# Performance work log

Hardware: AMD Instinct MI355X
Metric: run time of the kernel (lower is better)

The kernel has to match this reference:

```python
import jax, jax.numpy as jnp
import numpy as np
import math

D_MODEL = 1024
D_STATE = 16
D_CONV = 4
EXPAND = 2
D_INNER = EXPAND * D_MODEL  # 2048
DT_RANK = 64
B_SZ = 2
L_SEQ = 1024


def setup_inputs() -> dict:
    key = jax.random.key(0)
    ks = jax.random.split(key, 10)
    x = jax.random.normal(ks[0], (B_SZ, L_SEQ, D_MODEL), dtype=jnp.float32)
    in_proj_w = jax.random.normal(ks[1], (2 * D_INNER, D_MODEL), dtype=jnp.float32) * (1.0 / math.sqrt(D_MODEL))
    conv_w = jax.random.normal(ks[2], (D_INNER, 1, D_CONV), dtype=jnp.float32) * (1.0 / math.sqrt(D_CONV))
    conv_b = jax.random.normal(ks[3], (D_INNER,), dtype=jnp.float32) * 0.01
    x_proj_w = jax.random.normal(ks[4], (DT_RANK + 2 * D_STATE, D_INNER), dtype=jnp.float32) * (1.0 / math.sqrt(D_INNER))
    dt_init_std = DT_RANK ** (-0.5)
    dt_proj_w = jax.random.uniform(ks[5], (D_INNER, DT_RANK), dtype=jnp.float32, minval=-dt_init_std, maxval=dt_init_std)
    dt = jnp.exp(jax.random.uniform(ks[6], (D_INNER,), dtype=jnp.float32) * (math.log(0.1) - math.log(0.001)) + math.log(0.001))
    dt = jnp.clip(dt, 1e-4, None)
    dt_proj_b = dt + jnp.log(-jnp.expm1(-dt))
    A_log = jnp.log(jnp.tile(jnp.arange(1, D_STATE + 1, dtype=jnp.float32)[None, :], (D_INNER, 1)))
    D = jnp.ones((D_INNER,), dtype=jnp.float32)
    out_proj_w = jax.random.normal(ks[7], (D_MODEL, D_INNER), dtype=jnp.float32) * (1.0 / math.sqrt(D_INNER))
    return {"x": x, "in_proj_w": in_proj_w, "conv_w": conv_w, "conv_b": conv_b,
            "x_proj_w": x_proj_w, "dt_proj_w": dt_proj_w, "dt_proj_b": dt_proj_b,
            "A_log": A_log, "D": D, "out_proj_w": out_proj_w}


def _mamba_forward(x, in_proj_w, conv_w, conv_b, x_proj_w, dt_proj_w, dt_proj_b, A_log, D, out_proj_w):
    B, L, _ = x.shape
    # input projection -> x, z each [B, L, Di]
    xz = jnp.einsum('bld,ed->ble', x, in_proj_w)
    xs, z = jnp.split(xz, 2, axis=-1)
    # causal depthwise conv along L (torch pads K-1 both sides then trims -> left pad only)
    xc = jnp.transpose(xs, (0, 2, 1))  # [B, Di, L]
    xc = jax.lax.conv_general_dilated(
        xc, conv_w, window_strides=(1,), padding=[(D_CONV - 1, 0)],
        feature_group_count=D_INNER, dimension_numbers=('NCH', 'OIH', 'NCH'))
    xc = xc + conv_b[None, :, None]
    xs = jnp.transpose(xc, (0, 2, 1))  # [B, L, Di]
    xs = jax.nn.silu(xs)
    # SSM parameters
    A = -jnp.exp(A_log)  # [Di, N]
    dbc = jnp.einsum('bld,ed->ble', xs, x_proj_w)
    delta_r = dbc[..., :DT_RANK]
    Bm = dbc[..., DT_RANK:DT_RANK + D_STATE]       # [B, L, N]
    Cm = dbc[..., DT_RANK + D_STATE:]              # [B, L, N]
    delta = jnp.einsum('blr,dr->bld', delta_r, dt_proj_w)
    delta = jax.nn.softplus(delta + dt_proj_b)     # [B, L, Di]
    # selective scan: h_t = exp(delta*A)*h_{t-1} + delta*B*x
    dA = jnp.exp(delta[..., None] * A)                          # [B, L, Di, N]
    dBx = (delta * xs)[..., None] * Bm[:, :, None, :]           # [B, L, Di, N]
    dA_t = jnp.moveaxis(dA, 1, 0)    # [L, B, Di, N]
    dBx_t = jnp.moveaxis(dBx, 1, 0)
    C_t = jnp.moveaxis(Cm, 1, 0)     # [L, B, N]
    h0 = jnp.zeros((B, D_INNER, D_STATE), dtype=xs.dtype)

    def step(h, inp):
        da, bx, c = inp
        h = da * h + bx
        y = jnp.einsum('bdn,bn->bd', h, c)
        return h, y

    _, ys = jax.lax.scan(step, h0, (dA_t, dBx_t, C_t))
    y = jnp.moveaxis(ys, 0, 1)       # [B, L, Di]
    y = y + D * xs
    # gating and output projection
    out = y * jax.nn.silu(z)
    return jnp.einsum('bld,od->blo', out, out_proj_w)


def reference(x, in_proj_w, conv_w, conv_b, x_proj_w, dt_proj_w, dt_proj_b, A_log, D, out_proj_w):
    return _mamba_forward(x, in_proj_w, conv_w, conv_b, x_proj_w, dt_proj_w, dt_proj_b, A_log, D, out_proj_w)
```

## Files before the change

### kernel.cpp

```cpp
#include <hip/hip_runtime.h>
#include <hip/hip_bf16.h>

typedef __attribute__((ext_vector_type(8))) short short8;
typedef __attribute__((ext_vector_type(4))) float f32x4;
typedef __hip_bfloat16 bf16;

#define D_MODEL 1024
#define D_INNER 2048
#define DT_RANK 64
#define D_STATE 16
#define B_SZ 2
#define L_SEQ 1024
#define NSEG 32
#define SL 32

__device__ __forceinline__ float b2f(bf16 x){ return __bfloat162float(x); }
__device__ __forceinline__ bf16  f2b(float x){ return __float2bfloat16(x); }

__device__ __forceinline__ void cvt_store8(bf16* dst, const float* s){
  union { short8 v; bf16 e[8]; } u;
  #pragma unroll
  for (int i = 0; i < 8; i++) u.e[i] = f2b(s[i]);
  *(short8*)dst = u.v;
}

__device__ __forceinline__ void gl_lds16(const bf16* g, bf16* l){
  __builtin_amdgcn_global_load_lds((const __attribute__((address_space(1))) unsigned int*)g,
                                   (__attribute__((address_space(3))) unsigned int*)l, 16, 0, 0);
}

__global__ __launch_bounds__(256) void cvt5_k(const float* s0, bf16* d0, int c0,
                                              const float* s1, bf16* d1, int c1,
                                              const float* s2, bf16* d2, int c2,
                                              const float* s3, bf16* d3, int c3,
                                              const float* s4, bf16* d4, int c4)
{
  int i = blockIdx.x * 256 + threadIdx.x;
  const float* s; bf16* d; int off;
  if      (i < c0) { s = s0; d = d0; off = i; }
  else if (i < c1) { s = s1; d = d1; off = i - c0; }
  else if (i < c2) { s = s2; d = d2; off = i - c1; }
  else if (i < c3) { s = s3; d = d3; off = i - c2; }
  else if (i < c4) { s = s4; d = d4; off = i - c3; }
  else return;
  float b[8];
  *(float4*)&b[0] = *(const float4*)(s + (size_t)off * 8);
  *(float4*)&b[4] = *(const float4*)(s + (size_t)off * 8 + 4);
  cvt_store8(d + (size_t)off * 8, b);
}

template<int MODE, int JT, int SPLITK>
__global__ __launch_bounds__(256) void gemm_glds(const bf16* __restrict__ A,
                                                 const bf16* __restrict__ B,
                                                 void* __restrict__ Cout,
                                                 int M, int N, int K)
{
  constexpr int BN = JT * 32;
  constexpr int BI = BN / 64;
  __shared__ bf16 As[128 * 32];
  __shared__ bf16 Bs[BN * 32];

  const int gx = gridDim.x;
  const int nwg = gx * gridDim.y;
  const int flat = blockIdx.y * gx + blockIdx.x;
  const int swz = (flat & 7) * (nwg >> 3) + (flat >> 3);
  const int bm = (swz / gx) * 128, bn = (swz % gx) * BN;

  const int Kc = K / SPLITK;
  const int kb = (SPLITK > 1) ? blockIdx.z * Kc : 0;

  const int tid  = threadIdx.x;
  const int lane = tid & 63, wave = tid >> 6;
  const int wm = (wave & 1) * 64, wn = (wave >> 1) * (JT * 16);
  const int r = lane & 15, q = lane >> 4;

  const bf16* asrc[2];
  #pragma unroll
  for (int i = 0; i < 2; i++) {
    int c = i * 256 + tid;
    asrc[i] = A + (size_t)(bm + (c >> 2)) * K + kb + (c & 3) * 8;
  }
  const bf16* bsrc[BI];
  #pragma unroll
  for (int i = 0; i < BI; i++) {
    int c = i * 256 + tid;
    bsrc[i] = B + (size_t)(bn + (c >> 2)) * K + kb + (c & 3) * 8;
  }

  f32x4 acc[4][JT];
  #pragma unroll
  for (int i = 0; i < 4; i++)
    #pragma unroll
    for (int j = 0; j < JT; j++) acc[i][j] = (f32x4){0.f,0.f,0.f,0.f};

  for (int k0 = 0; k0 < Kc; k0 += 32) {
    #pragma unroll
    for (int i = 0; i < 2; i++)
      gl_lds16(asrc[i] + k0, &As[(i * 256 + tid) * 8]);
    #pragma unroll
    for (int i = 0; i < BI; i++)
      gl_lds16(bsrc[i] + k0, &Bs[(i * 256 + tid) * 8]);
    __syncthreads();
    short8 af[4], bfr[JT];
    #pragma unroll
    for (int i = 0; i < 4; i++)  af[i]  = *(const short8*)&As[(wm + i*16 + r) * 32 + q*8];
    #pragma unroll
    for (int j = 0; j < JT; j++) bfr[j] = *(const short8*)&Bs[(wn + j*16 + r) * 32 + q*8];
    #pragma unroll
    for (int j = 0; j < JT; j++)
      #pragma unroll
      for (int i = 0; i < 4; i++)
        acc[i][j] = __builtin_amdgcn_mfma_f32_16x16x32_bf16(af[i], bfr[j], acc[i][j], 0, 0, 0);
    __syncthreads();
  }

  float* outf = (float*)Cout + (size_t)((SPLITK > 1) ? blockIdx.z : 0) * M * N;
  #pragma unroll
  for (int i = 0; i < 4; i++)
    #pragma unroll
    for (int j = 0; j < JT; j++)
      #pragma unroll
      for (int t = 0; t < 4; t++) {
        int row = bm + wm + i*16 + q*4 + t;
        int col = bn + wn + j*16 + r;
        float v = acc[i][j][t];
        if (MODE == 0) outf[(size_t)row * N + col] = v;
        else           ((bf16*)Cout)[(size_t)row * N + col] = f2b(v);
      }
}

__global__ __launch_bounds__(256) void addout_k(const float* __restrict__ p,
                                                float* __restrict__ out, int n4)
{
  int i = blockIdx.x * 256 + threadIdx.x;
  float4 a = ((const float4*)p)[i];
  float4 b = ((const float4*)p)[(size_t)i + n4];
  float4 o; o.x = a.x + b.x; o.y = a.y + b.y; o.z = a.z + b.z; o.w = a.w + b.w;
  ((float4*)out)[i] = o;
}

__global__ __launch_bounds__(256) void gemm_dt(const bf16* __restrict__ A,
                                               const bf16* __restrict__ W,
                                               float* __restrict__ Cout,
                                               const float* __restrict__ bias,
                                               int M, int N)
{
  __shared__ __align__(16) float stg[4][16][68];
  const int lane = threadIdx.x & 63, wave = threadIdx.x >> 6;
  const int ntg  = N >> 6;
  const int task = blockIdx.x * 4 + wave;
  const int mt   = task / ntg;
  const int ng   = task - mt * ntg;
  const int r = lane & 15, q = lane >> 4;

  const bf16* pa = A + (size_t)(mt*16 + r) * DT_RANK + q*8;
  short8 a0 = *(const short8*)pa;
  short8 a1 = *(const short8*)(pa + 32);

  #pragma unroll
  for (int j = 0; j < 4; j++) {
    const bf16* pb = W + (size_t)(ng*64 + j*16 + r) * DT_RANK + q*8;
    short8 b0 = *(const short8*)pb;
    short8 b1 = *(const short8*)(pb + 32);
    f32x4 c = {0.f,0.f,0.f,0.f};
    c = __builtin_amdgcn_mfma_f32_16x16x32_bf16(a0, b0, c, 0, 0, 0);
    c = __builtin_amdgcn_mfma_f32_16x16x32_bf16(a1, b1, c, 0, 0, 0);
    float bv = bias[ng*64 + j*16 + r];
    #pragma unroll
    for (int t = 0; t < 4; t++) {
      float xv = c[t] + bv;
      float sp = (xv > 20.f) ? xv : log1pf(__expf(xv));
      stg[wave][q*4 + t][j*16 + r] = sp;
    }
  }
  {
    int row = lane >> 2, q4 = lane & 3;
    const float* src = &stg[wave][row][q4 * 16];
    float4 w0 = *(const float4*)(src);
    float4 w1 = *(const float4*)(src + 4);
    float4 w2 = *(const float4*)(src + 8);
    float4 w3 = *(const float4*)(src + 12);
    float* gdst = Cout + (size_t)(mt*16 + row) * N + ng*64 + q4*16;
    *(float4*)(gdst)      = w0;
    *(float4*)(gdst + 4)  = w1;
    *(float4*)(gdst + 8)  = w2;
    *(float4*)(gdst + 12) = w3;
  }
}

__global__ __launch_bounds__(256) void gemm_xproj(const bf16* __restrict__ A,
                                                  const bf16* __restrict__ W,
                                                  float* __restrict__ dbc,
                                                  bf16* __restrict__ dr)
{
  const int K = D_INNER;
  const int lane = threadIdx.x & 63, wave = threadIdx.x >> 6;
  const int mt = blockIdx.y * 4 + wave;
  const int nt = blockIdx.x;
  const int r = lane & 15, q = lane >> 4;
  const bf16* pa = A + (size_t)(mt*16 + r) * K + q*8;
  const bf16* pb = W + (size_t)(nt*16 + r) * K + q*8;
  f32x4 a0 = {0.f,0.f,0.f,0.f}, a1 = a0, a2 = a0, a3 = a0;
  for (int k0 = 0; k0 < K; k0 += 128) {
    short8 x0 = *(const short8*)(pa + k0);
    short8 w0 = *(const short8*)(pb + k0);
    short8 x1 = *(const short8*)(pa + k0 + 32);
    short8 w1 = *(const short8*)(pb + k0 + 32);
    short8 x2 = *(const short8*)(pa + k0 + 64);
    short8 w2 = *(const short8*)(pb + k0 + 64);
    short8 x3 = *(const short8*)(pa + k0 + 96);
    short8 w3 = *(const short8*)(pb + k0 + 96);
    a0 = __builtin_amdgcn_mfma_f32_16x16x32_bf16(x0, w0, a0, 0, 0, 0);
    a1 = __builtin_amdgcn_mfma_f32_16x16x32_bf16(x1, w1, a1, 0, 0, 0);
    a2 = __builtin_amdgcn_mfma_f32_16x16x32_bf16(x2, w2, a2, 0, 0, 0);
    a3 = __builtin_amdgcn_mfma_f32_16x16x32_bf16(x3, w3, a3, 0, 0, 0);
  }
  f32x4 acc = (a0 + a1) + (a2 + a3);
  #pragma unroll
  for (int t = 0; t < 4; t++) {
    int row = mt*16 + q*4 + t;
    int col = nt*16 + r;
    dbc[(size_t)row * 96 + col] = acc[t];
    if (col < DT_RANK) dr[(size_t)row * DT_RANK + col] = f2b(acc[t]);
  }
}

__global__ __launch_bounds__(256) void conv_silu_k(const bf16* __restrict__ xz,
                                                   const float* __restrict__ cw,
                                                   const float* __restrict__ cb,
                                                   bf16* __restrict__ xs_b)
{
  int idx = blockIdx.x * 256 + threadIdx.x;
  int dg = idx & (D_INNER/8 - 1);
  int bl = idx >> 8;
  int l  = bl & (L_SEQ - 1);
  int d0 = dg * 8;
  const float4* cw4 = (const float4*)cw;
  float4 w[8];
  #pragma unroll
  for (int i = 0; i < 8; i++) w[i] = cw4[d0 + i];
  float acc[8];
  #pragma unroll
  for (int i = 0; i < 8; i++) acc[i] = cb[d0 + i];
  #pragma unroll
  for (int j = 0; j < 4; ++j) {
    int lp = l - 3 + j;
    if (lp >= 0) {
      short8 v = *(const short8*)(xz + (size_t)(bl - 3 + j) * (2*D_INNER) + d0);
      #pragma unroll
      for (int i = 0; i < 8; i++)
        acc[i] += ((const float*)&w[i])[j] * b2f(((const bf16*)&v)[i]);
    }
  }
  float o[8];
  #pragma unroll
  for (int i = 0; i < 8; i++) o[i] = acc[i] / (1.f + __expf(-acc[i]));
  cvt_store8(xs_b + (size_t)idx * 8, o);
}

__global__ __launch_bounds__(256) void scan_pass1(const float* __restrict__ delta,
                                                  const bf16* __restrict__ xs,
                                                  const float* __restrict__ dbc,
                                                  const float* __restrict__ A_log,
                                                  float* __restrict__ hseg,
                                                  float* __restrict__ Stot)
{
  __shared__ float bcs[SL][32];
  const int d   = blockIdx.x * 256 + threadIdx.x;
  const int seg = blockIdx.y, b = blockIdx.z;
  for (int i = threadIdx.x; i < SL*32; i += 256) {
    int l = i >> 5, c = i & 31;
    bcs[l][c] = dbc[((size_t)b*L_SEQ + seg*SL + l)*96 + DT_RANK + c];
  }
  __syncthreads();
  float An[16], h[16];
  #pragma unroll
  for (int n = 0; n < 16; n++) { An[n] = -__expf(A_log[d*16 + n]); h[n] = 0.f; }
  float S = 0.f;
  for (int li = 0; li < SL; ++li) {
    size_t bl = (size_t)b * L_SEQ + seg*SL + li;
    float dv = delta[bl*D_INNER + d];
    float xv = b2f(xs[bl*D_INNER + d]);
    S += dv;
    float dx = dv * xv;
    #pragma unroll
    for (int n = 0; n < 16; n++)
      h[n] = __expf(dv * An[n]) * h[n] + dx * bcs[li][n];
  }
  float* hp = hseg + (((size_t)seg*B_SZ + b)*D_INNER + d) * 16;
  #pragma unroll
  for (int n = 0; n < 16; n++) hp[n] = h[n];
  Stot[((size_t)seg*B_SZ + b)*D_INNER + d] = S;
}

__global__ __launch_bounds__(256) void scan_combine(const float* __restrict__ Stot,
                                                    float* __restrict__ hseg,
                                                    const float* __restrict__ A_log)
{
  int idx = blockIdx.x * 256 + threadIdx.x;
  int n = idx & 15;
  int d = (idx >> 4) & (D_INNER - 1);
  int b = idx >> 15;
  float An = -__expf(A_log[d*16 + n]);
  float H = 0.f;
  for (int s = 0; s < NSEG; s++) {
    size_t base = ((size_t)s*B_SZ + b)*D_INNER + d;
    float St   = Stot[base];
    float hloc = hseg[base*16 + n];
    hseg[base*16 + n] = H;
    H = __expf(An*St)*H + hloc;
  }
}

__global__ __launch_bounds__(256) void scan_pass3(const float* __restrict__ delta,
                                                  const bf16* __restrict__ xs,
                                                  const float* __restrict__ dbc,
                                                  const float* __restrict__ A_log,
                                                  const float* __restrict__ hseg,
                                                  const bf16* __restrict__ xz,
                                                  const float* __restrict__ Dw,
                                                  bf16* __restrict__ outin)
{
  __shared__ float bcs[SL][32];
  const int d   = blockIdx.x * 256 + threadIdx.x;
  const int seg = blockIdx.y, b = blockIdx.z;
  for (int i = threadIdx.x; i < SL*32; i += 256) {
    int l = i >> 5, c = i & 31;
    bcs[l][c] = dbc[((size_t)b*L_SEQ + seg*SL + l)*96 + DT_RANK + c];
  }
  __syncthreads();
  float An[16], h[16];
  const float* hp = hseg + (((size_t)seg*B_SZ + b)*D_INNER + d) * 16;
  #pragma unroll
  for (int n = 0; n < 16; n++) { An[n] = -__expf(A_log[d*16 + n]); h[n] = hp[n]; }
  const float Dv = Dw[d];
  for (int li = 0; li < SL; ++li) {
    size_t bl = (size_t)b * L_SEQ + seg*SL + li;
    float dv = delta[bl*D_INNER + d];
    float xv = b2f(xs[bl*D_INNER + d]);
    float dx = dv * xv;
    float y = 0.f;
    #pragma unroll
    for (int n = 0; n < 16; n++) {
      h[n] = __expf(dv * An[n]) * h[n] + dx * bcs[li][n];
      y   += h[n] * bcs[li][16 + n];
    }
    y += Dv * xv;
    float z = b2f(xz[bl*(size_t)(2*D_INNER) + D_INNER + d]);
    float g = z / (1.f + __expf(-z));
    outin[bl*D_INNER + d] = f2b(y * g);
  }
}

extern "C" void kernel_launch(void* const* d_in, const int* in_sizes, int n_in,
                              void* d_out, int out_size, void* d_ws, size_t ws_size,
                              hipStream_t stream)
{
  const float* x      = (const float*)d_in[0];
  const float* in_w   = (const float*)d_in[1];
  const float* conv_w = (const float*)d_in[2];
  const float* conv_b = (const float*)d_in[3];
  const float* xp_w   = (const float*)d_in[4];
  const float* dt_w   = (const float*)d_in[5];
  const float* dt_b   = (const float*)d_in[6];
  const float* A_log  = (const float*)d_in[7];
  const float* Dw     = (const float*)d_in[8];
  const float* out_w  = (const float*)d_in[9];
  float* out = (float*)d_out;

  char* p = (char*)d_ws;
  bf16*  xz    = (bf16*)p;  p += (size_t)B_SZ*L_SEQ*2*D_INNER*2;
  bf16*  xs_b  = (bf16*)p;  p += (size_t)B_SZ*L_SEQ*D_INNER*2;
  float* dbc   = (float*)p; p += (size_t)B_SZ*L_SEQ*96*4;
  bf16*  dr    = (bf16*)p;  p += (size_t)B_SZ*L_SEQ*DT_RANK*2;
  float* delta = (float*)p; p += (size_t)B_SZ*L_SEQ*D_INNER*4;
  float* Stot  = (float*)p; p += (size_t)NSEG*B_SZ*D_INNER*4;
  bf16*  outin = (bf16*)p;  p += (size_t)B_SZ*L_SEQ*D_INNER*2;
  bf16*  xp_wb = (bf16*)p;  p += (size_t)(DT_RANK+2*D_STATE)*D_INNER*2;
  bf16*  dt_wb = (bf16*)p;  p += (size_t)D_INNER*DT_RANK*2;
  bf16*  ow_b  = (bf16*)p;  p += (size_t)D_MODEL*D_INNER*2;
  float* out_p = (float*)p; p += (size_t)2*B_SZ*L_SEQ*D_MODEL*4;
  char* u = p;
  bf16*  xb    = (bf16*)u;
  bf16*  in_wb = (bf16*)(u + (size_t)B_SZ*L_SEQ*D_MODEL*2);
  float* hseg  = (float*)u;
  p += (size_t)B_SZ*L_SEQ*(D_MODEL + 2*D_INNER)*2;

  const int M = B_SZ * L_SEQ;

  cvt5_k<<<4256, 256, 0, stream>>>(x, xb, 262144,
                                   in_w, in_wb, 786432,
                                   xp_w, xp_wb, 811008,
                                   dt_w, dt_wb, 827392,
                                   out_w, ow_b, 1089536);
  gemm_glds<2,2,1><<<dim3(2*D_INNER/64, M/128, 1), 256, 0, stream>>>(xb, in_wb, xz, M, 2*D_INNER, D_MODEL);
  conv_silu_k<<<(M*D_INNER/8)/256, 256, 0, stream>>>(xz, conv_w, conv_b, xs_b);
  gemm_xproj<<<dim3(6, M/64), 256, 0, stream>>>(xs_b, xp_wb, dbc, dr);
  gemm_dt<<<(M/16)*(D_INNER/64)/4, 256, 0, stream>>>(dr, dt_wb, delta, dt_b, M, D_INNER);
  scan_pass1<<<dim3(D_INNER/256, NSEG, B_SZ), 256, 0, stream>>>(delta, xs_b, dbc, A_log, hseg, Stot);
  scan_combine<<<(B_SZ*D_INNER*16)/256, 256, 0, stream>>>(Stot, hseg, A_log);
  scan_pass3<<<dim3(D_INNER/256, NSEG, B_SZ), 256, 0, stream>>>(delta, xs_b, dbc, A_log, hseg, xz, Dw, outin);
  gemm_glds<0,2,2><<<dim3(D_MODEL/64, M/128, 2), 256, 0, stream>>>(outin, ow_b, out_p, M, D_MODEL, D_INNER);
  addout_k<<<(M*D_MODEL/4)/256, 256, 0, stream>>>(out_p, out, M*D_MODEL/4);
}
```

Before: 261.4 us.

## Specialise scan for integer A via power recurrence and drop split-K output GEMM

Adds a runtime check in both scan passes: when A equals -(n+1) for each state, the per-state decay is computed as successive powers of exp(-delta), replacing sixteen exponentials per step with one exponential and multiplies. The general path remains as a fallback. The output projection GEMM no longer uses split-K with a separate reduction kernel; it writes results directly, saving a partial buffer and an extra pass but halving the grid size. The power recurrence may accumulate slightly more rounding error than direct exponentials.

```diff
diff --git a/kernel.cpp b/kernel.cpp
--- a/kernel.cpp
+++ b/kernel.cpp
@@ -49,7 +49,7 @@
   cvt_store8(d + (size_t)off * 8, b);
 }
 
-template<int MODE, int JT, int SPLITK>
+template<int MODE, int JT>
 __global__ __launch_bounds__(256) void gemm_glds(const bf16* __restrict__ A,
                                                  const bf16* __restrict__ B,
                                                  void* __restrict__ Cout,
@@ -66,9 +66,6 @@
   const int swz = (flat & 7) * (nwg >> 3) + (flat >> 3);
   const int bm = (swz / gx) * 128, bn = (swz % gx) * BN;
 
-  const int Kc = K / SPLITK;
-  const int kb = (SPLITK > 1) ? blockIdx.z * Kc : 0;
-
   const int tid  = threadIdx.x;
   const int lane = tid & 63, wave = tid >> 6;
   const int wm = (wave & 1) * 64, wn = (wave >> 1) * (JT * 16);
@@ -78,13 +75,13 @@
   #pragma unroll
   for (int i = 0; i < 2; i++) {
     int c = i * 256 + tid;
-    asrc[i] = A + (size_t)(bm + (c >> 2)) * K + kb + (c & 3) * 8;
+    asrc[i] = A + (size_t)(bm + (c >> 2)) * K + (c & 3) * 8;
   }
   const bf16* bsrc[BI];
   #pragma unroll
   for (int i = 0; i < BI; i++) {
     int c = i * 256 + tid;
-    bsrc[i] = B + (size_t)(bn + (c >> 2)) * K + kb + (c & 3) * 8;
+    bsrc[i] = B + (size_t)(bn + (c >> 2)) * K + (c & 3) * 8;
   }
 
   f32x4 acc[4][JT];
@@ -93,7 +90,7 @@
     #pragma unroll
     for (int j = 0; j < JT; j++) acc[i][j] = (f32x4){0.f,0.f,0.f,0.f};
 
-  for (int k0 = 0; k0 < Kc; k0 += 32) {
+  for (int k0 = 0; k0 < K; k0 += 32) {
     #pragma unroll
     for (int i = 0; i < 2; i++)
       gl_lds16(asrc[i] + k0, &As[(i * 256 + tid) * 8]);
@@ -114,7 +111,6 @@
     __syncthreads();
   }
 
-  float* outf = (float*)Cout + (size_t)((SPLITK > 1) ? blockIdx.z : 0) * M * N;
   #pragma unroll
   for (int i = 0; i < 4; i++)
     #pragma unroll
@@ -124,19 +120,9 @@
         int row = bm + wm + i*16 + q*4 + t;
         int col = bn + wn + j*16 + r;
         float v = acc[i][j][t];
-        if (MODE == 0) outf[(size_t)row * N + col] = v;
+        if (MODE == 0) ((float*)Cout)[(size_t)row * N + col] = v;
         else           ((bf16*)Cout)[(size_t)row * N + col] = f2b(v);
       }
-}
-
-__global__ __launch_bounds__(256) void addout_k(const float* __restrict__ p,
-                                                float* __restrict__ out, int n4)
-{
-  int i = blockIdx.x * 256 + threadIdx.x;
-  float4 a = ((const float4*)p)[i];
-  float4 b = ((const float4*)p)[(size_t)i + n4];
-  float4 o; o.x = a.x + b.x; o.y = a.y + b.y; o.z = a.z + b.z; o.w = a.w + b.w;
-  ((float4*)out)[i] = o;
 }
 
 __global__ __launch_bounds__(256) void gemm_dt(const bf16* __restrict__ A,
@@ -258,6 +244,13 @@
   cvt_store8(xs_b + (size_t)idx * 8, o);
 }
 
+__device__ __forceinline__ bool an_is_int(const float* An){
+  bool f = true;
+  #pragma unroll
+  for (int n = 0; n < 16; n++) f = f & (fabsf(An[n] + (float)(n+1)) < 1e-3f);
+  return f;
+}
+
 __global__ __launch_bounds__(256) void scan_pass1(const float* __restrict__ delta,
                                                   const bf16* __restrict__ xs,
                                                   const float* __restrict__ dbc,
@@ -277,15 +270,31 @@
   #pragma unroll
   for (int n = 0; n < 16; n++) { An[n] = -__expf(A_log[d*16 + n]); h[n] = 0.f; }
   float S = 0.f;
-  for (int li = 0; li < SL; ++li) {
-    size_t bl = (size_t)b * L_SEQ + seg*SL + li;
-    float dv = delta[bl*D_INNER + d];
-    float xv = b2f(xs[bl*D_INNER + d]);
-    S += dv;
-    float dx = dv * xv;
-    #pragma unroll
-    for (int n = 0; n < 16; n++)
-      h[n] = __expf(dv * An[n]) * h[n] + dx * bcs[li][n];
+  if (an_is_int(An)) {
+    for (int li = 0; li < SL; ++li) {
+      size_t bl = (size_t)b * L_SEQ + seg*SL + li;
+      float dv = delta[bl*D_INNER + d];
+      float xv = b2f(xs[bl*D_INNER + d]);
+      S += dv;
+      float dx = dv * xv;
+      float q = __expf(-dv), w = 1.f;
+      #pragma unroll
+      for (int n = 0; n < 16; n++) {
+        w *= q;
+        h[n] = w * h[n] + dx * bcs[li][n];
+      }
+    }
+  } else {
+    for (int li = 0; li < SL; ++li) {
+      size_t bl = (size_t)b * L_SEQ + seg*SL + li;
+      float dv = delta[bl*D_INNER + d];
+      float xv = b2f(xs[bl*D_INNER + d]);
+      S += dv;
+      float dx = dv * xv;
+      #pragma unroll
+      for (int n = 0; n < 16; n++)
+        h[n] = __expf(dv * An[n]) * h[n] + dx * bcs[li][n];
+    }
   }
   float* hp = hseg + (((size_t)seg*B_SZ + b)*D_INNER + d) * 16;
   #pragma unroll
@@ -334,21 +343,42 @@
   #pragma unroll
   for (int n = 0; n < 16; n++) { An[n] = -__expf(A_log[d*16 + n]); h[n] = hp[n]; }
   const float Dv = Dw[d];
-  for (int li = 0; li < SL; ++li) {
-    size_t bl = (size_t)b * L_SEQ + seg*SL + li;
-    float dv = delta[bl*D_INNER + d];
-    float xv = b2f(xs[bl*D_INNER + d]);
-    float dx = dv * xv;
-    float y = 0.f;
-    #pragma unroll
-    for (int n = 0; n < 16; n++) {
-      h[n] = __expf(dv * An[n]) * h[n] + dx * bcs[li][n];
-      y   += h[n] * bcs[li][16 + n];
-    }
-    y += Dv * xv;
-    float z = b2f(xz[bl*(size_t)(2*D_INNER) + D_INNER + d]);
-    float g = z / (1.f + __expf(-z));
-    outin[bl*D_INNER + d] = f2b(y * g);
+  if (an_is_int(An)) {
+    for (int li = 0; li < SL; ++li) {
+      size_t bl = (size_t)b * L_SEQ + seg*SL + li;
+      float dv = delta[bl*D_INNER + d];
+      float xv = b2f(xs[bl*D_INNER + d]);
+      float dx = dv * xv;
+      float q = __expf(-dv), w = 1.f;
+      float y = 0.f;
+      #pragma unroll
+      for (int n = 0; n < 16; n++) {
+        w *= q;
+        h[n] = w * h[n] + dx * bcs[li][n];
+        y   += h[n] * bcs[li][16 + n];
+      }
+      y += Dv * xv;
+      float z = b2f(xz[bl*(size_t)(2*D_INNER) + D_INNER + d]);
+      float g = z / (1.f + __expf(-z));
+      outin[bl*D_INNER + d] = f2b(y * g);
+    }
+  } else {
+    for (int li = 0; li < SL; ++li) {
+      size_t bl = (size_t)b * L_SEQ + seg*SL + li;
+      float dv = delta[bl*D_INNER + d];
+      float xv = b2f(xs[bl*D_INNER + d]);
+      float dx = dv * xv;
+      float y = 0.f;
+      #pragma unroll
+      for (int n = 0; n < 16; n++) {
+        h[n] = __expf(dv * An[n]) * h[n] + dx * bcs[li][n];
+        y   += h[n] * bcs[li][16 + n];
+      }
+      y += Dv * xv;
+      float z = b2f(xz[bl*(size_t)(2*D_INNER) + D_INNER + d]);
+      float g = z / (1.f + __expf(-z));
+      outin[bl*D_INNER + d] = f2b(y * g);
+    }
   }
 }
 
@@ -379,7 +409,6 @@
   bf16*  xp_wb = (bf16*)p;  p += (size_t)(DT_RANK+2*D_STATE)*D_INNER*2;
   bf16*  dt_wb = (bf16*)p;  p += (size_t)D_INNER*DT_RANK*2;
   bf16*  ow_b  = (bf16*)p;  p += (size_t)D_MODEL*D_INNER*2;
-  float* out_p = (float*)p; p += (size_t)2*B_SZ*L_SEQ*D_MODEL*4;
   char* u = p;
   bf16*  xb    = (bf16*)u;
   bf16*  in_wb = (bf16*)(u + (size_t)B_SZ*L_SEQ*D_MODEL*2);
@@ -393,13 +422,12 @@
                                    xp_w, xp_wb, 811008,
                                    dt_w, dt_wb, 827392,
                                    out_w, ow_b, 1089536);
-  gemm_glds<2,2,1><<<dim3(2*D_INNER/64, M/128, 1), 256, 0, stream>>>(xb, in_wb, xz, M, 2*D_INNER, D_MODEL);
+  gemm_glds<2,2><<<dim3(2*D_INNER/64, M/128), 256, 0, stream>>>(xb, in_wb, xz, M, 2*D_INNER, D_MODEL);
   conv_silu_k<<<(M*D_INNER/8)/256, 256, 0, stream>>>(xz, conv_w, conv_b, xs_b);
   gemm_xproj<<<dim3(6, M/64), 256, 0, stream>>>(xs_b, xp_wb, dbc, dr);
   gemm_dt<<<(M/16)*(D_INNER/64)/4, 256, 0, stream>>>(dr, dt_wb, delta, dt_b, M, D_INNER);
   scan_pass1<<<dim3(D_INNER/256, NSEG, B_SZ), 256, 0, stream>>>(delta, xs_b, dbc, A_log, hseg, Stot);
   scan_combine<<<(B_SZ*D_INNER*16)/256, 256, 0, stream>>>(Stot, hseg, A_log);
   scan_pass3<<<dim3(D_INNER/256, NSEG, B_SZ), 256, 0, stream>>>(delta, xs_b, dbc, A_log, hseg, xz, Dw, outin);
-  gemm_glds<0,2,2><<<dim3(D_MODEL/64, M/128, 2), 256, 0, stream>>>(outin, ow_b, out_p, M, D_MODEL, D_INNER);
-  addout_k<<<(M*D_MODEL/4)/256, 256, 0, stream>>>(out_p, out, M*D_MODEL/4);
-}
+  gemm_glds<0,2><<<dim3(D_MODEL/64, M/128), 256, 0, stream>>>(outin, ow_b, out, M, D_MODEL, D_INNER);
+}
```

Measured after the change: 255.3 us. -2.3%, faster.
